# Optimization experiments

Measured on AMD Instinct MI355X. Metric: run time of the kernel, lower is better.

The kernel has to match this reference:

```python
import jax, jax.numpy as jnp
import numpy as np

ITERATIONS = 3
OUT_CAPS, OUT_DIM = 10, 16


def squash(x):
    # square_norm / (1 + square_norm) * x / (sqrt(square_norm) + 1e-6), norm over last axis
    sn = jnp.sum(x * x, axis=-1, keepdims=True)
    return sn / (1.0 + sn) * x / (jnp.sqrt(sn) + 1e-6)


def setup_inputs() -> dict:
    key = jax.random.key(0)
    kx, kw = jax.random.split(key)
    x = jax.random.normal(kx, (256, 32, 6, 6, 8), dtype=jnp.float32)
    W = 0.01 * jax.random.normal(kw, (1, 32, 6, 6, 10, 8, 16), dtype=jnp.float32)
    return {"x": x, "W": W}


def reference(x, W):
    w = W[0]  # [i,j,k,o,d,e]
    # u_hat: prediction vectors, [B, i, j, k, O, E]
    u_hat = jnp.einsum('bijkd,ijkode->bijkoe', x, w)
    u_det = jax.lax.stop_gradient(u_hat)
    b = jnp.zeros(u_hat.shape[:-1], dtype=u_hat.dtype)  # [B,i,j,k,O]
    for _ in range(ITERATIONS - 1):
        c = jax.nn.softmax(b, axis=-1)
        s = jnp.einsum('bijko,bijkoe->boe', c, u_det)   # reduce over all input-capsule axes
        v = squash(s)                                    # [B,O,E]
        b = b + jnp.einsum('bijkoe,boe->bijko', u_det, v)
    c = jax.nn.softmax(b, axis=-1)
    s = jnp.einsum('bijko,bijkoe->boe', c, u_hat)
    v = squash(s)
    return v.reshape(-1, OUT_CAPS, OUT_DIM)
```

## Files before the change

### kernel.cpp

```cpp
#include <hip/hip_runtime.h>
#include <math.h>

#define BATCH 256
#define IC    1152
#define DD    8
#define OO    10
#define EE    16
#define BTILE 64
#define NBT   4
#define NT    640
#define CHUNK 18
#define NCHUNK 64
#define SJ    3
#define ROUNDS (CHUNK / SJ)

__global__ __launch_bounds__(NT) void caps_pass_kernel(
    const float* __restrict__ x,
    const float* __restrict__ W,
    const float* __restrict__ V,
    float* __restrict__ s_part,
    int first)
{
    __shared__ float x_lds[2][SJ][DD][BTILE];
    __shared__ float logit_lds[2][SJ][NT];

    const int tid = threadIdx.x;
    const int o   = tid >> 6;
    const int bl  = tid & 63;
    const int o_u = __builtin_amdgcn_readfirstlane(o);
    const int b   = blockIdx.y * BTILE + bl;
    const int ijk0 = blockIdx.x * CHUNK;

    float vreg[EE];
    if (first) {
        #pragma unroll
        for (int e = 0; e < EE; ++e) vreg[e] = 0.f;
    } else {
        const float4* vp = reinterpret_cast<const float4*>(V + ((size_t)b * OO + o) * EE);
        #pragma unroll
        for (int q = 0; q < 4; ++q) {
            float4 t = vp[q];
            vreg[q * 4 + 0] = t.x; vreg[q * 4 + 1] = t.y;
            vreg[q * 4 + 2] = t.z; vreg[q * 4 + 3] = t.w;
        }
    }

    float sacc[EE];
    #pragma unroll
    for (int e = 0; e < EE; ++e) sacc[e] = 0.f;

    const bool loader = tid < SJ * BTILE * 2;
    const int ls = tid >> 7;
    const int lr = tid & 127;
    const int lb = lr >> 1;
    const int lq = lr & 1;
    const float* xbase = x + (size_t)(blockIdx.y * BTILE + lb) * (IC * DD) + lq * 4;

    float4 xpre = make_float4(0.f, 0.f, 0.f, 0.f);
    if (loader) xpre = *reinterpret_cast<const float4*>(xbase + (size_t)(ijk0 + ls) * DD);
    if (loader) {
        x_lds[0][ls][lq * 4 + 0][lb] = xpre.x;
        x_lds[0][ls][lq * 4 + 1][lb] = xpre.y;
        x_lds[0][ls][lq * 4 + 2][lb] = xpre.z;
        x_lds[0][ls][lq * 4 + 3][lb] = xpre.w;
    }
    __syncthreads();

    int p = 0;
    for (int r = 0; r < ROUNDS; ++r) {
        if (r + 1 < ROUNDS && loader)
            xpre = *reinterpret_cast<const float4*>(
                xbase + (size_t)(ijk0 + (r + 1) * SJ + ls) * DD);

        float u[SJ][EE];
        float lgr[SJ];
        #pragma unroll
        for (int s = 0; s < SJ; ++s) {
            const int ijk = ijk0 + r * SJ + s;
            const float* wp = W + (size_t)ijk * (OO * DD * EE) + o_u * (DD * EE);
            float xr[DD];
            #pragma unroll
            for (int d = 0; d < DD; ++d) xr[d] = x_lds[p][s][d][bl];
            #pragma unroll
            for (int e = 0; e < EE; ++e) u[s][e] = 0.f;
            #pragma unroll
            for (int d = 0; d < DD; ++d) {
                #pragma unroll
                for (int e = 0; e < EE; ++e)
                    u[s][e] = fmaf(xr[d], wp[d * EE + e], u[s][e]);
            }
            if (!first) {
                float lg = 0.f;
                #pragma unroll
                for (int e = 0; e < EE; ++e) lg += u[s][e] * vreg[e];
                lgr[s] = lg;
                logit_lds[p][s][tid] = lg;
            }
        }

        if (r + 1 < ROUNDS && loader) {
            x_lds[p ^ 1][ls][lq * 4 + 0][lb] = xpre.x;
            x_lds[p ^ 1][ls][lq * 4 + 1][lb] = xpre.y;
            x_lds[p ^ 1][ls][lq * 4 + 2][lb] = xpre.z;
            x_lds[p ^ 1][ls][lq * 4 + 3][lb] = xpre.w;
        }

        __syncthreads();

        if (first) {
            #pragma unroll
            for (int s = 0; s < SJ; ++s)
                #pragma unroll
                for (int e = 0; e < EE; ++e) sacc[e] += 0.1f * u[s][e];
        } else {
            #pragma unroll
            for (int s = 0; s < SJ; ++s) {
                float m = -1e30f;
                #pragma unroll
                for (int oo = 0; oo < OO; ++oo)
                    m = fmaxf(m, logit_lds[p][s][oo * 64 + bl]);
                float den = 0.f;
                #pragma unroll
                for (int oo = 0; oo < OO; ++oo)
                    den += __expf(logit_lds[p][s][oo * 64 + bl] - m);
                float c = __expf(lgr[s] - m) / den;
                #pragma unroll
                for (int e = 0; e < EE; ++e) sacc[e] += c * u[s][e];
            }
        }
        p ^= 1;
    }

    float* sp = s_part + (((size_t)blockIdx.x * BATCH + b) * OO + o) * EE;
    #pragma unroll
    for (int q = 0; q < 4; ++q) {
        float4 t;
        t.x = sacc[q * 4 + 0]; t.y = sacc[q * 4 + 1];
        t.z = sacc[q * 4 + 2]; t.w = sacc[q * 4 + 3];
        reinterpret_cast<float4*>(sp)[q] = t;
    }
}

__global__ __launch_bounds__(256) void caps_squash_kernel(
    const float* __restrict__ s_part,
    float* __restrict__ V,
    float* __restrict__ out,
    int accum, int last)
{
    const int g = blockIdx.x * 256 + threadIdx.x;
    float s = 0.f;
    for (int ch = 0; ch < NCHUNK; ++ch)
        s += s_part[(size_t)ch * (BATCH * OO * EE) + g];

    float sq = s * s;
    #pragma unroll
    for (int m = 1; m < 16; m <<= 1) sq += __shfl_xor(sq, m, 16);

    float scale = sq / (1.f + sq) / (sqrtf(sq) + 1e-6f);
    float v = scale * s;

    if (last)       out[g] = v;
    else if (accum) V[g]  += v;
    else            V[g]   = v;
}

extern "C" void kernel_launch(void* const* d_in, const int* in_sizes, int n_in,
                              void* d_out, int out_size, void* d_ws, size_t ws_size,
                              hipStream_t stream) {
    const float* x = (const float*)d_in[0];
    const float* W = (const float*)d_in[1];
    float* out = (float*)d_out;

    float* s_part = (float*)d_ws;
    float* V      = s_part + (size_t)NCHUNK * BATCH * OO * EE;

    dim3 grid(NCHUNK, NBT), blk(NT);
    const int sq_blocks = (BATCH * OO * EE) / 256;

    caps_pass_kernel<<<grid, blk, 0, stream>>>(x, W, V, s_part, 1);
    caps_squash_kernel<<<sq_blocks, 256, 0, stream>>>(s_part, V, out, 0, 0);
    caps_pass_kernel<<<grid, blk, 0, stream>>>(x, W, V, s_part, 0);
    caps_squash_kernel<<<sq_blocks, 256, 0, stream>>>(s_part, V, out, 1, 0);
    caps_pass_kernel<<<grid, blk, 0, stream>>>(x, W, V, s_part, 0);
    caps_squash_kernel<<<sq_blocks, 256, 0, stream>>>(s_part, V, out, 0, 1);
}
```

Before: 159.5 us.

## Halve chunk size, drop x LDS staging, skip softmax max, parallelize squash reduction

The input-capsule chunk is halved to double the grid and add parallelism, with occupancy hinted through launch bounds. Each thread now loads its x vector directly from global memory instead of through a double-buffered LDS stage. The first pass drops its barriers entirely. The softmax skips max subtraction by exponentiating the logits directly, which assumes the logits stay small enough not to overflow. The squash kernel splits the now-longer chunk reduction across four waves with an LDS combine, at the cost of twice the partial-sum traffic.

```diff
diff --git a/kernel.cpp b/kernel.cpp
--- a/kernel.cpp
+++ b/kernel.cpp
@@ -9,20 +9,19 @@
 #define BTILE 64
 #define NBT   4
 #define NT    640
-#define CHUNK 18
-#define NCHUNK 64
+#define CHUNK 9
+#define NCHUNK 128
 #define SJ    3
 #define ROUNDS (CHUNK / SJ)
 
-__global__ __launch_bounds__(NT) void caps_pass_kernel(
+__global__ __launch_bounds__(NT, 5) void caps_pass_kernel(
     const float* __restrict__ x,
     const float* __restrict__ W,
     const float* __restrict__ V,
     float* __restrict__ s_part,
     int first)
 {
-    __shared__ float x_lds[2][SJ][DD][BTILE];
-    __shared__ float logit_lds[2][SJ][NT];
+    __shared__ float elg_lds[2][SJ][NT];
 
     const int tid = threadIdx.x;
     const int o   = tid >> 6;
@@ -31,11 +30,10 @@
     const int b   = blockIdx.y * BTILE + bl;
     const int ijk0 = blockIdx.x * CHUNK;
 
+    const float* xb = x + (size_t)b * (IC * DD);
+
     float vreg[EE];
-    if (first) {
-        #pragma unroll
-        for (int e = 0; e < EE; ++e) vreg[e] = 0.f;
-    } else {
+    if (!first) {
         const float4* vp = reinterpret_cast<const float4*>(V + ((size_t)b * OO + o) * EE);
         #pragma unroll
         for (int q = 0; q < 4; ++q) {
@@ -49,38 +47,19 @@
     #pragma unroll
     for (int e = 0; e < EE; ++e) sacc[e] = 0.f;
 
-    const bool loader = tid < SJ * BTILE * 2;
-    const int ls = tid >> 7;
-    const int lr = tid & 127;
-    const int lb = lr >> 1;
-    const int lq = lr & 1;
-    const float* xbase = x + (size_t)(blockIdx.y * BTILE + lb) * (IC * DD) + lq * 4;
-
-    float4 xpre = make_float4(0.f, 0.f, 0.f, 0.f);
-    if (loader) xpre = *reinterpret_cast<const float4*>(xbase + (size_t)(ijk0 + ls) * DD);
-    if (loader) {
-        x_lds[0][ls][lq * 4 + 0][lb] = xpre.x;
-        x_lds[0][ls][lq * 4 + 1][lb] = xpre.y;
-        x_lds[0][ls][lq * 4 + 2][lb] = xpre.z;
-        x_lds[0][ls][lq * 4 + 3][lb] = xpre.w;
-    }
-    __syncthreads();
-
     int p = 0;
     for (int r = 0; r < ROUNDS; ++r) {
-        if (r + 1 < ROUNDS && loader)
-            xpre = *reinterpret_cast<const float4*>(
-                xbase + (size_t)(ijk0 + (r + 1) * SJ + ls) * DD);
-
         float u[SJ][EE];
-        float lgr[SJ];
+        float elg[SJ];
         #pragma unroll
         for (int s = 0; s < SJ; ++s) {
             const int ijk = ijk0 + r * SJ + s;
             const float* wp = W + (size_t)ijk * (OO * DD * EE) + o_u * (DD * EE);
+            const float4 x0 = *reinterpret_cast<const float4*>(xb + (size_t)ijk * DD);
+            const float4 x1 = *reinterpret_cast<const float4*>(xb + (size_t)ijk * DD + 4);
             float xr[DD];
-            #pragma unroll
-            for (int d = 0; d < DD; ++d) xr[d] = x_lds[p][s][d][bl];
+            xr[0] = x0.x; xr[1] = x0.y; xr[2] = x0.z; xr[3] = x0.w;
+            xr[4] = x1.x; xr[5] = x1.y; xr[6] = x1.z; xr[7] = x1.w;
             #pragma unroll
             for (int e = 0; e < EE; ++e) u[s][e] = 0.f;
             #pragma unroll
@@ -93,50 +72,40 @@
                 float lg = 0.f;
                 #pragma unroll
                 for (int e = 0; e < EE; ++e) lg += u[s][e] * vreg[e];
-                lgr[s] = lg;
-                logit_lds[p][s][tid] = lg;
+                elg[s] = __expf(lg);
+                elg_lds[p][s][tid] = elg[s];
             }
         }
 
-        if (r + 1 < ROUNDS && loader) {
-            x_lds[p ^ 1][ls][lq * 4 + 0][lb] = xpre.x;
-            x_lds[p ^ 1][ls][lq * 4 + 1][lb] = xpre.y;
-            x_lds[p ^ 1][ls][lq * 4 + 2][lb] = xpre.z;
-            x_lds[p ^ 1][ls][lq * 4 + 3][lb] = xpre.w;
-        }
-
-        __syncthreads();
-
-        if (first) {
+        if (!first) {
+            __syncthreads();
+            #pragma unroll
+            for (int s = 0; s < SJ; ++s) {
+                float den = 0.f;
+                #pragma unroll
+                for (int oo = 0; oo < OO; ++oo)
+                    den += elg_lds[p][s][oo * 64 + bl];
+                float c = __fdividef(elg[s], den);
+                #pragma unroll
+                for (int e = 0; e < EE; ++e)
+                    sacc[e] = fmaf(c, u[s][e], sacc[e]);
+            }
+            p ^= 1;
+        } else {
             #pragma unroll
             for (int s = 0; s < SJ; ++s)
                 #pragma unroll
-                for (int e = 0; e < EE; ++e) sacc[e] += 0.1f * u[s][e];
-        } else {
-            #pragma unroll
-            for (int s = 0; s < SJ; ++s) {
-                float m = -1e30f;
-                #pragma unroll
-                for (int oo = 0; oo < OO; ++oo)
-                    m = fmaxf(m, logit_lds[p][s][oo * 64 + bl]);
-                float den = 0.f;
-                #pragma unroll
-                for (int oo = 0; oo < OO; ++oo)
-                    den += __expf(logit_lds[p][s][oo * 64 + bl] - m);
-                float c = __expf(lgr[s] - m) / den;
-                #pragma unroll
-                for (int e = 0; e < EE; ++e) sacc[e] += c * u[s][e];
-            }
+                for (int e = 0; e < EE; ++e) sacc[e] += u[s][e];
         }
-        p ^= 1;
     }
 
+    const float mul = first ? 0.1f : 1.0f;
     float* sp = s_part + (((size_t)blockIdx.x * BATCH + b) * OO + o) * EE;
     #pragma unroll
     for (int q = 0; q < 4; ++q) {
         float4 t;
-        t.x = sacc[q * 4 + 0]; t.y = sacc[q * 4 + 1];
-        t.z = sacc[q * 4 + 2]; t.w = sacc[q * 4 + 3];
+        t.x = mul * sacc[q * 4 + 0]; t.y = mul * sacc[q * 4 + 1];
+        t.z = mul * sacc[q * 4 + 2]; t.w = mul * sacc[q * 4 + 3];
         reinterpret_cast<float4*>(sp)[q] = t;
     }
 }
@@ -147,21 +116,33 @@
     float* __restrict__ out,
     int accum, int last)
 {
-    const int g = blockIdx.x * 256 + threadIdx.x;
+    __shared__ float red[3][64];
+    const int lane = threadIdx.x & 63;
+    const int w    = threadIdx.x >> 6;
+    const int g    = blockIdx.x * 64 + lane;
+
+    const float* sp = s_part + g;
     float s = 0.f;
-    for (int ch = 0; ch < NCHUNK; ++ch)
-        s += s_part[(size_t)ch * (BATCH * OO * EE) + g];
+    #pragma unroll 8
+    for (int ch = w * (NCHUNK / 4); ch < (w + 1) * (NCHUNK / 4); ++ch)
+        s += sp[(size_t)ch * (BATCH * OO * EE)];
 
-    float sq = s * s;
-    #pragma unroll
-    for (int m = 1; m < 16; m <<= 1) sq += __shfl_xor(sq, m, 16);
+    if (w > 0) red[w - 1][lane] = s;
+    __syncthreads();
+    if (w == 0) {
+        s += red[0][lane] + red[1][lane] + red[2][lane];
 
-    float scale = sq / (1.f + sq) / (sqrtf(sq) + 1e-6f);
-    float v = scale * s;
+        float sq = s * s;
+        #pragma unroll
+        for (int m = 1; m < 16; m <<= 1) sq += __shfl_xor(sq, m, 16);
 
-    if (last)       out[g] = v;
-    else if (accum) V[g]  += v;
-    else            V[g]   = v;
+        float scale = sq / (1.f + sq) / (sqrtf(sq) + 1e-6f);
+        float v = scale * s;
+
+        if (last)       out[g] = v;
+        else if (accum) V[g]  += v;
+        else            V[g]   = v;
+    }
 }
 
 extern "C" void kernel_launch(void* const* d_in, const int* in_sizes, int n_in,
@@ -175,7 +156,7 @@
     float* V      = s_part + (size_t)NCHUNK * BATCH * OO * EE;
 
     dim3 grid(NCHUNK, NBT), blk(NT);
-    const int sq_blocks = (BATCH * OO * EE) / 256;
+    const int sq_blocks = (BATCH * OO * EE) / 64;
 
     caps_pass_kernel<<<grid, blk, 0, stream>>>(x, W, V, s_part, 1);
     caps_squash_kernel<<<sq_blocks, 256, 0, stream>>>(s_part, V, out, 0, 0);
```

New measurement: 209.0 us. +31.0%, slower.
